# Optimization experiments

Hardware: AMD Instinct MI355X
Metric: run time of the kernel (lower is better)

Reference implementation:

```python
import jax, jax.numpy as jnp
import numpy as np
from math import log

N = 100000          # num_nodes
D = 128             # emb_dimension
NEG = 5             # negatives per node
LR = 0.025
NCE_BIAS = log(N)
NCE_NEG_BIAS = log(N / NEG)
LUT_SIZE = 1202     # len(arange(-6.01, 6.01, 0.01))


def make_lookup_table():
    t = jax.nn.sigmoid(jnp.arange(-6.01, 6.01, 0.01, dtype=jnp.float32))
    t = t.at[0].set(0.0).at[-1].set(1.0)
    return t


def fast_sigmoid(score, lookup_table):
    idx = jnp.floor((score + 6.01) / 0.01).astype(jnp.int32)
    idx = jnp.clip(idx, 0, LUT_SIZE - 1)  # guard float rounding at +/-6
    return jnp.take(lookup_table, idx)


def setup_inputs() -> dict:
    key = jax.random.key(0)
    k1, k2, k3, k4, k5 = jax.random.split(key, 5)
    W = jax.random.uniform(k1, (N, D), dtype=jnp.float32, minval=-0.5, maxval=0.5)
    lookup_table = make_lookup_table()
    idx_pos_u = jax.random.randint(k2, (N,), 0, N)
    idx_pos_v = jax.random.randint(k3, (N,), 0, N)
    idx_neg_u = jnp.repeat(idx_pos_u, NEG)  # matches sample_index: same u repeated per negative
    idx_neg_v = jax.random.randint(k5, (N * NEG,), 0, N)
    return {"W": W, "lookup_table": lookup_table,
            "idx_pos_u": idx_pos_u, "idx_pos_v": idx_pos_v,
            "idx_neg_u": idx_neg_u, "idx_neg_v": idx_neg_v}


def reference(W, lookup_table, idx_pos_u, idx_pos_v, idx_neg_u, idx_neg_v):
    # ---- positive pairs: gather, dot, LUT-sigmoid, scatter-add ----
    emb_pos_u = W[idx_pos_u]                       # [N, D]
    emb_pos_v = W[idx_pos_v]                       # [N, D]
    pos_score = jnp.sum(emb_pos_u * emb_pos_v, axis=1) - NCE_BIAS
    pos_score = jnp.clip(pos_score, -6.0, 6.0)
    score = ((1.0 - fast_sigmoid(pos_score, lookup_table)) * LR)[:, None]
    W = W.at[idx_pos_u].add(score * emb_pos_v)
    W = W.at[idx_pos_v].add(score * emb_pos_u)
    # ---- negative pairs: gathers read the UPDATED table (as in torch code) ----
    emb_neg_u = W[idx_neg_u]                       # [N*NEG, D]
    emb_neg_v = W[idx_neg_v]                       # [N*NEG, D]
    neg_score = jnp.sum(emb_neg_u * emb_neg_v, axis=1) - NCE_NEG_BIAS
    neg_score = jnp.clip(neg_score, -6.0, 6.0)
    score = (0.0 - fast_sigmoid(neg_score, lookup_table) * LR)[:, None]
    W = W.at[idx_neg_u].add(score * emb_neg_v)
    W = W.at[idx_neg_v].add(score * emb_neg_u)
    return W
```

## Files before the change

### kernel.cpp

```cpp
#include <hip/hip_runtime.h>
#include <hip/hip_bf16.h>

#define D 128
#define LR 0.025f
#define NCE_BIAS 11.512925464970229f
#define NCE_NEG_BIAS 9.903487552536127f
#define LUT_SIZE 1202

__device__ __forceinline__ float wave_allreduce(float x) {
    #pragma unroll
    for (int m = 32; m >= 1; m >>= 1) x += __shfl_xor(x, m, 64);
    return x;
}

__device__ __forceinline__ float fast_sig(float x) {
    x = fminf(fmaxf(x, -6.0f), 6.0f) - 0.005f;
    float e = __expf(-x);
    return __builtin_amdgcn_rcpf(1.0f + e);
}

__device__ __forceinline__ float fast_sig_lut(float s, const float* __restrict__ lut) {
    s = fminf(fmaxf(s, -6.0f), 6.0f);
    int idx = (int)floorf((s + 6.01f) / 0.01f);
    idx = min(max(idx, 0), LUT_SIZE - 1);
    return lut[idx];
}

__device__ __forceinline__ unsigned int bf16_rne(float f) {
    unsigned int u = __float_as_uint(f);
    return (u + 0x7FFFu + ((u >> 16) & 1u)) >> 16;
}

__global__ __launch_bounds__(256) void conv_kernel(
    const float* __restrict__ W, unsigned short* __restrict__ w16, int n32)
{
    int g = blockIdx.x * 256 + threadIdx.x;
    if (g >= n32) return;
    float4 v = ((const float4*)W)[g];
    uint2 h;
    h.x = bf16_rne(v.x) | (bf16_rne(v.y) << 16);
    h.y = bf16_rne(v.z) | (bf16_rne(v.w) << 16);
    ((uint2*)w16)[g] = h;
}

__global__ __launch_bounds__(256) void hist_kernel(
    const int* __restrict__ ipu, const int* __restrict__ ipv,
    const int* __restrict__ inv,
    int Np, int Nn, int NEG, int2* __restrict__ cnt2)
{
    int t = blockIdx.x * 256 + threadIdx.x;
    if (t < Np) {
        atomicAdd((unsigned long long*)&cnt2[ipu[t]],
                  1ull + ((unsigned long long)NEG << 32));
        atomicAdd(&cnt2[ipv[t]].x, 1);
    } else if (t < Np + Nn) {
        int k = t - Np;
        atomicAdd(&cnt2[inv[k]].y, 1);
    }
}

__global__ __launch_bounds__(256) void scan_local2(
    const int2* __restrict__ cnt2, int* __restrict__ off_p, int* __restrict__ off_n,
    int* __restrict__ bsp, int* __restrict__ bsn, int n)
{
    __shared__ int shp[256], shn[256];
    int g = blockIdx.x * 256 + threadIdx.x;
    int2 x = (g < n) ? cnt2[g] : make_int2(0, 0);
    shp[threadIdx.x] = x.x;
    shn[threadIdx.x] = x.y;
    __syncthreads();
    #pragma unroll
    for (int d = 1; d < 256; d <<= 1) {
        int tp = (threadIdx.x >= d) ? shp[threadIdx.x - d] : 0;
        int tn = (threadIdx.x >= d) ? shn[threadIdx.x - d] : 0;
        __syncthreads();
        shp[threadIdx.x] += tp;
        shn[threadIdx.x] += tn;
        __syncthreads();
    }
    if (g < n) {
        off_p[g] = shp[threadIdx.x] - x.x;
        off_n[g] = shn[threadIdx.x] - x.y;
    }
    if (threadIdx.x == 255) {
        bsp[blockIdx.x] = shp[255];
        bsn[blockIdx.x] = shn[255];
    }
}

__device__ __forceinline__ void scan_one(int* b, int nb) {
    __shared__ int sh[256];
    __shared__ int carry_s;
    if (threadIdx.x == 0) carry_s = 0;
    __syncthreads();
    for (int c = 0; c < nb; c += 256) {
        int i = c + threadIdx.x;
        int x = (i < nb) ? b[i] : 0;
        sh[threadIdx.x] = x;
        __syncthreads();
        for (int d = 1; d < 256; d <<= 1) {
            int t = (threadIdx.x >= d) ? sh[threadIdx.x - d] : 0;
            __syncthreads();
            sh[threadIdx.x] += t;
            __syncthreads();
        }
        int carry = carry_s;
        if (i < nb) b[i] = sh[threadIdx.x] - x + carry;
        __syncthreads();
        if (threadIdx.x == 0) carry_s = carry + sh[255];
        __syncthreads();
    }
}

__global__ __launch_bounds__(256) void scan_bsum2(int* __restrict__ bsp, int* __restrict__ bsn, int nb)
{
    scan_one(bsp, nb);
    __syncthreads();
    scan_one(bsn, nb);
}

__global__ __launch_bounds__(256) void add_base2(
    int* __restrict__ off_p, int* __restrict__ off_n, int2* __restrict__ cur2,
    const int* __restrict__ bsp, const int* __restrict__ bsn, int n)
{
    int g = blockIdx.x * 256 + threadIdx.x;
    if (g < n) {
        int vp = off_p[g] + bsp[blockIdx.x];
        int vn = off_n[g] + bsn[blockIdx.x];
        off_p[g] = vp;
        off_n[g] = vn;
        cur2[g] = make_int2(vp, vn);
    }
}

__global__ __launch_bounds__(256) void fill_kernel(
    const int* __restrict__ ipu, const int* __restrict__ ipv,
    const int* __restrict__ inu, const int* __restrict__ inv,
    int Np, int Nn, int NEG,
    int2* __restrict__ cur2, int* __restrict__ ent_p, int* __restrict__ ent_n)
{
    int t = blockIdx.x * 256 + threadIdx.x;
    if (t < Np) {
        int u = ipu[t], v = ipv[t];
        unsigned long long pk = atomicAdd((unsigned long long*)&cur2[u],
                                          1ull + ((unsigned long long)NEG << 32));
        int slot_pu = (int)(pk & 0xFFFFFFFFull);
        int slot_nu = (int)(pk >> 32);
        ent_p[slot_pu] = v;
        for (int j = 0; j < NEG; ++j)
            ent_n[slot_nu + j] = inv[(size_t)NEG * t + j];
        ent_p[atomicAdd(&cur2[v].x, 1)] = u;
    } else if (t < Np + Nn) {
        int k = t - Np;
        ent_n[atomicAdd(&cur2[inv[k]].y, 1)] = inu[k];
    }
}

template<bool EMIT16>
__global__ __launch_bounds__(256) void update_kernel(
    const float* __restrict__ baseSrc,
    const unsigned short* __restrict__ partnerH,
    float* __restrict__ dst, unsigned short* __restrict__ dst16,
    const int* __restrict__ offArr, const int* __restrict__ endArr2, int comp,
    const int* __restrict__ entries, int N, float bias, float cpos)
{
    int gtid = blockIdx.x * 256 + threadIdx.x;
    int node = gtid >> 5;
    int hl   = threadIdx.x & 31;
    if (node >= N) return;

    const bool b3 = (hl & 8) != 0;
    const bool b4 = (hl & 16) != 0;
    const int i_lane = (hl >> 3) & 3;

    float4 base = ((const float4*)baseSrc)[(size_t)node * 32 + hl];
    float ax = 0.0f, ay = 0.0f, az = 0.0f, aw = 0.0f;

    int beg = offArr[node];
    int len = endArr2[2 * node + comp] - beg;
    const uint2* ph = (const uint2*)partnerH;

    if (len > 0) {
        int gcount = (len + 3) >> 2;
        int en[4];
        uint2 rc[4];
        #pragma unroll
        for (int i = 0; i < 4; ++i) {
            int t = min(i, len - 1);
            rc[i] = ph[(size_t)entries[beg + t] * 32 + hl];
        }
        #pragma unroll
        for (int i = 0; i < 4; ++i) {
            int t = min(4 + i, len - 1);
            en[i] = entries[beg + t];
        }
        for (int g = 0; g < gcount; ++g) {
            uint2 rn[4];
            #pragma unroll
            for (int i = 0; i < 4; ++i) rn[i] = ph[(size_t)en[i] * 32 + hl];
            int en2[4];
            #pragma unroll
            for (int i = 0; i < 4; ++i) {
                int t = (g + 2) * 4 + i;
                t = (t < len) ? t : (len - 1);
                en2[i] = entries[beg + t];
            }
            float4 r[4];
            float d[4];
            #pragma unroll
            for (int i = 0; i < 4; ++i) {
                r[i].x = __uint_as_float(rc[i].x << 16);
                r[i].y = __uint_as_float(rc[i].x & 0xFFFF0000u);
                r[i].z = __uint_as_float(rc[i].y << 16);
                r[i].w = __uint_as_float(rc[i].y & 0xFFFF0000u);
                d[i] = r[i].x * base.x + r[i].y * base.y + r[i].z * base.z + r[i].w * base.w;
            }
            float y0 = b4 ? d[0] : d[2];
            float y1 = b4 ? d[1] : d[3];
            y0 = __shfl_xor(y0, 16, 64);
            y1 = __shfl_xor(y1, 16, 64);
            float pa = b4 ? (d[2] + y0) : (d[0] + y0);
            float pb = b4 ? (d[3] + y1) : (d[1] + y1);
            float y2 = b3 ? pa : pb;
            y2 = __shfl_xor(y2, 8, 64);
            float cc = b3 ? (pb + y2) : (pa + y2);
            cc += __shfl_xor(cc, 4, 64);
            cc += __shfl_xor(cc, 2, 64);
            cc += __shfl_xor(cc, 1, 64);

            float s = (g * 4 + i_lane < len)
                        ? (cpos - fast_sig(cc - bias)) * LR : 0.0f;

            float t8  = __shfl_xor(s, 8, 64);
            float t16 = __shfl_xor(s, 16, 64);
            float t24 = __shfl_xor(t8, 16, 64);
            float p  = b3 ? t8  : s;
            float q  = b3 ? s   : t8;
            float p2 = b3 ? t24 : t16;
            float q2 = b3 ? t16 : t24;
            float se[4];
            se[0] = b4 ? p2 : p;
            se[1] = b4 ? q2 : q;
            se[2] = b4 ? p  : p2;
            se[3] = b4 ? q  : q2;

            #pragma unroll
            for (int i = 0; i < 4; ++i) {
                ax += se[i] * r[i].x;
                ay += se[i] * r[i].y;
                az += se[i] * r[i].z;
                aw += se[i] * r[i].w;
            }
            #pragma unroll
            for (int i = 0; i < 4; ++i) { rc[i] = rn[i]; en[i] = en2[i]; }
        }
    }
    float4 o = make_float4(base.x + ax, base.y + ay, base.z + az, base.w + aw);
    ((float4*)dst)[(size_t)node * 32 + hl] = o;
    if (EMIT16) {
        uint2 h;
        h.x = bf16_rne(o.x) | (bf16_rne(o.y) << 16);
        h.y = bf16_rne(o.z) | (bf16_rne(o.w) << 16);
        ((uint2*)dst16)[(size_t)node * 32 + hl] = h;
    }
}

__global__ __launch_bounds__(256) void pos_kernel(
    const float* __restrict__ Worig, float* __restrict__ W,
    const float* __restrict__ lut,
    const int* __restrict__ idx_u, const int* __restrict__ idx_v, int n)
{
    int wave = (int)((blockIdx.x * blockDim.x + threadIdx.x) >> 6);
    int lane = threadIdx.x & 63;
    if (wave >= n) return;
    int u = idx_u[wave];
    int v = idx_v[wave];
    float2 eu = ((const float2*)(Worig + (size_t)u * D))[lane];
    float2 ev = ((const float2*)(Worig + (size_t)v * D))[lane];
    float dot = wave_allreduce(eu.x * ev.x + eu.y * ev.y);
    float s = (1.0f - fast_sig_lut(dot - NCE_BIAS, lut)) * LR;
    float* wu = W + (size_t)u * D;
    float* wv = W + (size_t)v * D;
    atomicAdd(&wu[2 * lane],     s * ev.x);
    atomicAdd(&wu[2 * lane + 1], s * ev.y);
    atomicAdd(&wv[2 * lane],     s * eu.x);
    atomicAdd(&wv[2 * lane + 1], s * eu.y);
}

__global__ __launch_bounds__(256) void neg_kernel(
    const float* __restrict__ Wsnap, float* __restrict__ W,
    const float* __restrict__ lut,
    const int* __restrict__ idx_u, const int* __restrict__ idx_v, int n, int neg)
{
    int wave = (int)((blockIdx.x * blockDim.x + threadIdx.x) >> 6);
    int lane = threadIdx.x & 63;
    if (wave >= n) return;
    int u = idx_u[wave * neg];
    float2 eu = ((const float2*)(Wsnap + (size_t)u * D))[lane];
    float dux = 0.0f, duy = 0.0f;
    for (int j = 0; j < neg; ++j) {
        int v = idx_v[wave * neg + j];
        float2 ev = ((const float2*)(Wsnap + (size_t)v * D))[lane];
        float dot = wave_allreduce(eu.x * ev.x + eu.y * ev.y);
        float s = -fast_sig_lut(dot - NCE_NEG_BIAS, lut) * LR;
        dux += s * ev.x;
        duy += s * ev.y;
        float* wv = W + (size_t)v * D;
        atomicAdd(&wv[2 * lane],     s * eu.x);
        atomicAdd(&wv[2 * lane + 1], s * eu.y);
    }
    float* wu = W + (size_t)u * D;
    atomicAdd(&wu[2 * lane],     dux);
    atomicAdd(&wu[2 * lane + 1], duy);
}

extern "C" void kernel_launch(void* const* d_in, const int* in_sizes, int n_in,
                              void* d_out, int out_size, void* d_ws, size_t ws_size,
                              hipStream_t stream) {
    const float* W   = (const float*)d_in[0];
    const float* lut = (const float*)d_in[1];
    const int* ipu   = (const int*)d_in[2];
    const int* ipv   = (const int*)d_in[3];
    const int* inu   = (const int*)d_in[4];
    const int* inv   = (const int*)d_in[5];
    float* out = (float*)d_out;

    const int N  = in_sizes[0] / D;
    const int Np = in_sizes[2];
    const int Nn = in_sizes[4];
    const int NEG = Nn / Np;
    const size_t WB = (size_t)N * D * sizeof(float);
    const int nb = (N + 255) / 256;
    const int n_entp = 2 * Np;
    const int n_entn = NEG * Np + Nn;

    size_t need = (size_t)N * D * 2 * 2
                + (size_t)n_entp * 4 + (size_t)n_entn * 4
                + (size_t)N * 8 * 2 + (size_t)N * 4 * 2
                + (size_t)nb * 4 * 2 + 64;

    if (ws_size >= need) {
        char* p = (char*)d_ws;
        unsigned short* w16W = (unsigned short*)p; p += (size_t)N * D * 2;
        unsigned short* w16P = (unsigned short*)p; p += (size_t)N * D * 2;
        int*  ent_p = (int*)p;  p += (size_t)n_entp * 4;
        int*  ent_n = (int*)p;  p += (size_t)n_entn * 4;
        int2* cnt2  = (int2*)p; p += (size_t)N * 8;
        int2* cur2  = (int2*)p; p += (size_t)N * 8;
        int*  off_p = (int*)p;  p += (size_t)N * 4;
        int*  off_n = (int*)p;  p += (size_t)N * 4;
        int*  bsp   = (int*)p;  p += (size_t)nb * 4;
        int*  bsn   = (int*)p;

        hipMemsetAsync(cnt2, 0, (size_t)N * 8, stream);
        int n32 = N * 32;
        conv_kernel<<<(n32 + 255) / 256, 256, 0, stream>>>(W, w16W, n32);
        int tot = Np + Nn;
        hist_kernel<<<(tot + 255) / 256, 256, 0, stream>>>(ipu, ipv, inv, Np, Nn, NEG, cnt2);
        scan_local2<<<nb, 256, 0, stream>>>(cnt2, off_p, off_n, bsp, bsn, N);
        scan_bsum2<<<1, 256, 0, stream>>>(bsp, bsn, nb);
        add_base2<<<nb, 256, 0, stream>>>(off_p, off_n, cur2, bsp, bsn, N);
        fill_kernel<<<(tot + 255) / 256, 256, 0, stream>>>(ipu, ipv, inu, inv, Np, Nn, NEG,
                                                           cur2, ent_p, ent_n);

        int ublocks = (n32 + 255) / 256;
        update_kernel<true><<<ublocks, 256, 0, stream>>>(
            W, w16W, out, w16P, off_p, (const int*)cur2, 0, ent_p, N, NCE_BIAS, 1.0f);
        update_kernel<false><<<ublocks, 256, 0, stream>>>(
            out, w16P, out, (unsigned short*)nullptr, off_n, (const int*)cur2, 1, ent_n,
            N, NCE_NEG_BIAS, 0.0f);
    } else {
        float* snap = (float*)d_ws;
        hipMemcpyAsync(out, W, WB, hipMemcpyDeviceToDevice, stream);
        int blocks = (Np * 64 + 255) / 256;
        pos_kernel<<<blocks, 256, 0, stream>>>(W, out, lut, ipu, ipv, Np);
        hipMemcpyAsync(snap, out, WB, hipMemcpyDeviceToDevice, stream);
        neg_kernel<<<blocks, 256, 0, stream>>>(snap, out, lut, inu, inv, Np, NEG);
    }
}
```

Before: 272.7 us.

## Fuse conversion with histogram and replace three-kernel scan with single-pass scan

Merges the bf16 conversion and histogram kernels into one launch by partitioning blocks. Replaces the three-kernel scan (local scan, block-sum scan, add base) with a single-pass scan where blocks take a ticket, publish their inclusive sums, and spin-wait on the sums of earlier blocks. This removes several kernel launches and their serialization gaps, at the cost of spin-wait traffic on the partials array and a reliance on ticket ordering to avoid deadlock.

```diff
diff --git a/kernel.cpp b/kernel.cpp
--- a/kernel.cpp
+++ b/kernel.cpp
@@ -31,40 +31,46 @@
     return (u + 0x7FFFu + ((u >> 16) & 1u)) >> 16;
 }
 
-__global__ __launch_bounds__(256) void conv_kernel(
-    const float* __restrict__ W, unsigned short* __restrict__ w16, int n32)
-{
-    int g = blockIdx.x * 256 + threadIdx.x;
-    if (g >= n32) return;
-    float4 v = ((const float4*)W)[g];
-    uint2 h;
-    h.x = bf16_rne(v.x) | (bf16_rne(v.y) << 16);
-    h.y = bf16_rne(v.z) | (bf16_rne(v.w) << 16);
-    ((uint2*)w16)[g] = h;
-}
-
-__global__ __launch_bounds__(256) void hist_kernel(
+__global__ __launch_bounds__(256) void convhist_kernel(
+    const float* __restrict__ W, unsigned short* __restrict__ w16, int n32, int cb,
     const int* __restrict__ ipu, const int* __restrict__ ipv,
     const int* __restrict__ inv,
     int Np, int Nn, int NEG, int2* __restrict__ cnt2)
 {
-    int t = blockIdx.x * 256 + threadIdx.x;
-    if (t < Np) {
-        atomicAdd((unsigned long long*)&cnt2[ipu[t]],
-                  1ull + ((unsigned long long)NEG << 32));
-        atomicAdd(&cnt2[ipv[t]].x, 1);
-    } else if (t < Np + Nn) {
-        int k = t - Np;
-        atomicAdd(&cnt2[inv[k]].y, 1);
-    }
-}
-
-__global__ __launch_bounds__(256) void scan_local2(
-    const int2* __restrict__ cnt2, int* __restrict__ off_p, int* __restrict__ off_n,
-    int* __restrict__ bsp, int* __restrict__ bsn, int n)
+    int b = blockIdx.x;
+    if (b < cb) {
+        int g = b * 256 + threadIdx.x;
+        if (g >= n32) return;
+        float4 v = ((const float4*)W)[g];
+        uint2 h;
+        h.x = bf16_rne(v.x) | (bf16_rne(v.y) << 16);
+        h.y = bf16_rne(v.z) | (bf16_rne(v.w) << 16);
+        ((uint2*)w16)[g] = h;
+    } else {
+        int t = (b - cb) * 256 + threadIdx.x;
+        if (t < Np) {
+            atomicAdd((unsigned long long*)&cnt2[ipu[t]],
+                      1ull + ((unsigned long long)NEG << 32));
+            atomicAdd(&cnt2[ipv[t]].x, 1);
+        } else if (t < Np + Nn) {
+            int k = t - Np;
+            atomicAdd(&cnt2[inv[k]].y, 1);
+        }
+    }
+}
+
+__global__ __launch_bounds__(256) void scan_fused(
+    const int2* __restrict__ cnt2,
+    int* __restrict__ off_p, int* __restrict__ off_n, int2* __restrict__ cur2,
+    unsigned long long* __restrict__ partials, int* __restrict__ ticket, int n)
 {
     __shared__ int shp[256], shn[256];
-    int g = blockIdx.x * 256 + threadIdx.x;
+    __shared__ int tkt_s;
+    if (threadIdx.x == 0) tkt_s = atomicAdd(ticket, 1);
+    __syncthreads();
+    const int t = tkt_s;
+
+    int g = t * 256 + threadIdx.x;
     int2 x = (g < n) ? cnt2[g] : make_int2(0, 0);
     shp[threadIdx.x] = x.x;
     shn[threadIdx.x] = x.y;
@@ -78,55 +84,42 @@
         shn[threadIdx.x] += tn;
         __syncthreads();
     }
+    int incP = shp[threadIdx.x];
+    int incN = shn[threadIdx.x];
+
+    if (threadIdx.x == 255) {
+        unsigned long long v = (unsigned long long)(unsigned int)(incP + 1)
+                             | ((unsigned long long)(unsigned int)incN << 32);
+        atomicExch(&partials[t], v);
+    }
+
+    int myP = 0, myN = 0;
+    for (int i = threadIdx.x; i < t; i += 256) {
+        unsigned long long v;
+        do {
+            v = atomicAdd(&partials[i], 0ull);
+        } while ((v & 0xFFFFFFFFull) == 0ull);
+        myP += (int)(v & 0xFFFFFFFFull) - 1;
+        myN += (int)(v >> 32);
+    }
+    __syncthreads();
+    shp[threadIdx.x] = myP;
+    shn[threadIdx.x] = myN;
+    __syncthreads();
+    #pragma unroll
+    for (int d = 128; d > 0; d >>= 1) {
+        if (threadIdx.x < d) {
+            shp[threadIdx.x] += shp[threadIdx.x + d];
+            shn[threadIdx.x] += shn[threadIdx.x + d];
+        }
+        __syncthreads();
+    }
+    const int baseP = shp[0];
+    const int baseN = shn[0];
+
     if (g < n) {
-        off_p[g] = shp[threadIdx.x] - x.x;
-        off_n[g] = shn[threadIdx.x] - x.y;
-    }
-    if (threadIdx.x == 255) {
-        bsp[blockIdx.x] = shp[255];
-        bsn[blockIdx.x] = shn[255];
-    }
-}
-
-__device__ __forceinline__ void scan_one(int* b, int nb) {
-    __shared__ int sh[256];
-    __shared__ int carry_s;
-    if (threadIdx.x == 0) carry_s = 0;
-    __syncthreads();
-    for (int c = 0; c < nb; c += 256) {
-        int i = c + threadIdx.x;
-        int x = (i < nb) ? b[i] : 0;
-        sh[threadIdx.x] = x;
-        __syncthreads();
-        for (int d = 1; d < 256; d <<= 1) {
-            int t = (threadIdx.x >= d) ? sh[threadIdx.x - d] : 0;
-            __syncthreads();
-            sh[threadIdx.x] += t;
-            __syncthreads();
-        }
-        int carry = carry_s;
-        if (i < nb) b[i] = sh[threadIdx.x] - x + carry;
-        __syncthreads();
-        if (threadIdx.x == 0) carry_s = carry + sh[255];
-        __syncthreads();
-    }
-}
-
-__global__ __launch_bounds__(256) void scan_bsum2(int* __restrict__ bsp, int* __restrict__ bsn, int nb)
-{
-    scan_one(bsp, nb);
-    __syncthreads();
-    scan_one(bsn, nb);
-}
-
-__global__ __launch_bounds__(256) void add_base2(
-    int* __restrict__ off_p, int* __restrict__ off_n, int2* __restrict__ cur2,
-    const int* __restrict__ bsp, const int* __restrict__ bsn, int n)
-{
-    int g = blockIdx.x * 256 + threadIdx.x;
-    if (g < n) {
-        int vp = off_p[g] + bsp[blockIdx.x];
-        int vn = off_n[g] + bsn[blockIdx.x];
+        int vp = incP - x.x + baseP;
+        int vn = incN - x.y + baseN;
         off_p[g] = vp;
         off_n[g] = vn;
         cur2[g] = make_int2(vp, vn);
@@ -336,8 +329,10 @@
 
     size_t need = (size_t)N * D * 2 * 2
                 + (size_t)n_entp * 4 + (size_t)n_entn * 4
-                + (size_t)N * 8 * 2 + (size_t)N * 4 * 2
-                + (size_t)nb * 4 * 2 + 64;
+                + (size_t)N * 8
+                + 16 + (size_t)nb * 8
+                + (size_t)N * 8 + (size_t)N * 4 * 2
+                + 64;
 
     if (ws_size >= need) {
         char* p = (char*)d_ws;
@@ -345,21 +340,23 @@
         unsigned short* w16P = (unsigned short*)p; p += (size_t)N * D * 2;
         int*  ent_p = (int*)p;  p += (size_t)n_entp * 4;
         int*  ent_n = (int*)p;  p += (size_t)n_entn * 4;
+        char* zbase = p;
         int2* cnt2  = (int2*)p; p += (size_t)N * 8;
+        int*  ticket = (int*)p; p += 16;
+        unsigned long long* partials = (unsigned long long*)p; p += (size_t)nb * 8;
+        size_t zbytes = (size_t)(p - zbase);
         int2* cur2  = (int2*)p; p += (size_t)N * 8;
         int*  off_p = (int*)p;  p += (size_t)N * 4;
-        int*  off_n = (int*)p;  p += (size_t)N * 4;
-        int*  bsp   = (int*)p;  p += (size_t)nb * 4;
-        int*  bsn   = (int*)p;
-
-        hipMemsetAsync(cnt2, 0, (size_t)N * 8, stream);
+        int*  off_n = (int*)p;
+
+        hipMemsetAsync(zbase, 0, zbytes, stream);
         int n32 = N * 32;
-        conv_kernel<<<(n32 + 255) / 256, 256, 0, stream>>>(W, w16W, n32);
+        int cb = (n32 + 255) / 256;
+        int hb = (Np + Nn + 255) / 256;
+        convhist_kernel<<<cb + hb, 256, 0, stream>>>(W, w16W, n32, cb,
+                                                     ipu, ipv, inv, Np, Nn, NEG, cnt2);
+        scan_fused<<<nb, 256, 0, stream>>>(cnt2, off_p, off_n, cur2, partials, ticket, N);
         int tot = Np + Nn;
-        hist_kernel<<<(tot + 255) / 256, 256, 0, stream>>>(ipu, ipv, inv, Np, Nn, NEG, cnt2);
-        scan_local2<<<nb, 256, 0, stream>>>(cnt2, off_p, off_n, bsp, bsn, N);
-        scan_bsum2<<<1, 256, 0, stream>>>(bsp, bsn, nb);
-        add_base2<<<nb, 256, 0, stream>>>(off_p, off_n, cur2, bsp, bsn, N);
         fill_kernel<<<(tot + 255) / 256, 256, 0, stream>>>(ipu, ipv, inu, inv, Np, Nn, NEG,
                                                            cur2, ent_p, ent_n);
 
```

New measurement: 271.4 us. About the same (-0.5%).
